# Kernel tuning notes

Measured on AMD Instinct MI355X. Metric: run time of the kernel, lower is better.

Reference implementation:

```python
import jax, jax.numpy as jnp
import numpy as np

N_FRUSTUMS = 14400  # n_splits_azi(360) * n_splits_pol(40)
N_POINTS = 2_000_000
N_CHANNELS = 8


def setup_inputs() -> dict:
    key = jax.random.key(0)
    k1, k2 = jax.random.split(key)
    pc = jax.random.normal(k1, (N_POINTS, N_CHANNELS), dtype=jnp.float32)
    i_frustum = jnp.sort(
        jax.random.randint(k2, (N_POINTS,), 0, N_FRUSTUMS)
    ).astype(jnp.int32)
    i_inv = jnp.arange(N_POINTS, dtype=jnp.int32)  # identity inverse permutation
    counts_padded = jnp.bincount(i_frustum, length=N_FRUSTUMS).astype(jnp.float32)
    return {
        "pc": pc,
        "i_frustum": i_frustum,
        "i_inv": i_inv,
        "counts_padded": counts_padded,
    }


def reference(pc, i_frustum, i_inv, counts_padded):
    """Faithful port of symmetrize_mean / symmetrize_std / symmetrize_max plus the
    gather-broadcast normalize (pc - mean[i_frustum][i_inv]) / std.

    pc:            [N, C] float point features
    i_frustum:     [N]   int point->frustum segment ids (sorted)
    i_inv:         [N]   int inverse permutation applied after gather
    counts_padded: [F]   float per-frustum point counts (0 for empty frustums)
    """
    n_frustums = counts_padded.shape[0]
    nonempty = counts_padded[:, None] != 0.0  # [F, 1]
    safe_counts = jnp.maximum(counts_padded, 1.0)[:, None]  # avoid div-by-zero

    # symmetrize_mean: scatter_add then divide where count != 0
    sums = jax.ops.segment_sum(pc, i_frustum, num_segments=n_frustums)  # [F, C]
    mean = jnp.where(nonempty, sums / safe_counts, sums)

    # symmetrize_std: scatter_add of squared deviation, divide, sqrt where > 0
    dev = pc - mean[i_frustum][i_inv]  # [N, C] gather-broadcast subtract
    var_sums = jax.ops.segment_sum(dev * dev, i_frustum, num_segments=n_frustums)
    var = jnp.where(nonempty, var_sums / safe_counts, var_sums)
    std = jnp.where(var > 0.0, jnp.sqrt(jnp.maximum(var, 0.0)), var)

    # symmetrize_max: scatter_reduce amax onto a zeros-initialized buffer
    # (include_self=True default in torch => result is max(0, segment max))
    frustum_max = jnp.zeros((n_frustums, pc.shape[1]), pc.dtype).at[i_frustum].max(pc)

    # gather-broadcast normalize (decorator_distance_to_mean style, with per-frustum std)
    std_g = std[i_frustum][i_inv]
    pc_norm = dev / jnp.where(std_g > 0.0, std_g, 1.0)

    return mean, std, frustum_max, pc_norm
```

## Files before the change

### kernel.cpp

```cpp
#include <hip/hip_runtime.h>

#define NCH 8
#define CACHE 8

typedef float v4f __attribute__((ext_vector_type(4)));

__device__ __forceinline__ void acc4(const float4& v, float4& sum, float4& sq, float4& mx) {
    sum.x += v.x; sq.x += v.x * v.x; mx.x = fmaxf(mx.x, v.x);
    sum.y += v.y; sq.y += v.y * v.y; mx.y = fmaxf(mx.y, v.y);
    sum.z += v.z; sq.z += v.z * v.z; mx.z = fmaxf(mx.z, v.z);
    sum.w += v.w; sq.w += v.w * v.w; mx.w = fmaxf(mx.w, v.w);
}

__device__ __forceinline__ v4f norm4(const float4& v, const float4& m, const float4& d) {
    v4f o;
    o.x = (v.x - m.x) * d.x;
    o.y = (v.y - m.y) * d.y;
    o.z = (v.z - m.z) * d.z;
    o.w = (v.w - m.w) * d.w;
    return o;
}

__device__ __forceinline__ int wave_lower_bound(const int* __restrict__ a, int n, int key,
                                                int lane) {
    int lo = 0, len = n;
    while (len > 64) {
        int step = (len + 63) >> 6;
        int p = lo + lane * step;
        int v = (p < lo + len) ? a[p] : 0x7fffffff;
        unsigned long long bal = __ballot(v < key);
        int cnt = __popcll(bal);
        if (cnt == 0) return lo;
        int nlo = lo + (cnt - 1) * step + 1;
        int nhi = lo + len;
        int cap = lo + cnt * step;
        if (cnt < 64 && cap < nhi) nhi = cap;
        lo = nlo; len = nhi - nlo;
    }
    int v = (lane < len) ? a[lo + lane] : 0x7fffffff;
    unsigned long long bal = __ballot(v < key);
    return lo + __popcll(bal);
}

__global__ __launch_bounds__(128) void k_fused(
    const float* __restrict__ pc, const int* __restrict__ i_frustum,
    const float* __restrict__ counts, int n, int F,
    float* __restrict__ out_mean, float* __restrict__ out_std,
    float* __restrict__ out_max, float* __restrict__ out_pcn)
{
    const int wid = (blockIdx.x * blockDim.x + threadIdx.x) >> 6;
    if (wid >= F) return;
    const int lane = threadIdx.x & 63;

    const int s = wave_lower_bound(i_frustum, n, wid, lane);
    const float cnt = counts[wid];
    const int e = s + (int)cnt;

    const float4* __restrict__ pc4 = reinterpret_cast<const float4*>(pc);
    v4f* __restrict__ out4 = reinterpret_cast<v4f*>(out_pcn);

    const int b = s * 2, E = e * 2;

    float4 sum = {0.f, 0.f, 0.f, 0.f};
    float4 sq  = {0.f, 0.f, 0.f, 0.f};
    float4 mx  = {0.f, 0.f, 0.f, 0.f};
    float4 c[CACHE];

    int k = b + lane;
    #pragma unroll
    for (int u = 0; u < CACHE; ++u) {
        if (k < E) { c[u] = pc4[k]; acc4(c[u], sum, sq, mx); }
        k += 64;
    }
    for (int kk = k; kk < E; kk += 64) { float4 v = pc4[kk]; acc4(v, sum, sq, mx); }

    #pragma unroll
    for (int m = 2; m <= 32; m <<= 1) {
        sum.x += __shfl_xor(sum.x, m, 64);
        sum.y += __shfl_xor(sum.y, m, 64);
        sum.z += __shfl_xor(sum.z, m, 64);
        sum.w += __shfl_xor(sum.w, m, 64);
        sq.x  += __shfl_xor(sq.x,  m, 64);
        sq.y  += __shfl_xor(sq.y,  m, 64);
        sq.z  += __shfl_xor(sq.z,  m, 64);
        sq.w  += __shfl_xor(sq.w,  m, 64);
        mx.x = fmaxf(mx.x, __shfl_xor(mx.x, m, 64));
        mx.y = fmaxf(mx.y, __shfl_xor(mx.y, m, 64));
        mx.z = fmaxf(mx.z, __shfl_xor(mx.z, m, 64));
        mx.w = fmaxf(mx.w, __shfl_xor(mx.w, m, 64));
    }

    const float invc = 1.0f / fmaxf(cnt, 1.0f);
    float4 mean, sd, dv;
    mean.x = sum.x * invc; mean.y = sum.y * invc; mean.z = sum.z * invc; mean.w = sum.w * invc;
    float vx = fmaxf(sq.x * invc - mean.x * mean.x, 0.0f);
    float vy = fmaxf(sq.y * invc - mean.y * mean.y, 0.0f);
    float vz = fmaxf(sq.z * invc - mean.z * mean.z, 0.0f);
    float vw = fmaxf(sq.w * invc - mean.w * mean.w, 0.0f);
    sd.x = sqrtf(vx); sd.y = sqrtf(vy); sd.z = sqrtf(vz); sd.w = sqrtf(vw);
    dv.x = 1.0f / (sd.x > 0.f ? sd.x : 1.f);
    dv.y = 1.0f / (sd.y > 0.f ? sd.y : 1.f);
    dv.z = 1.0f / (sd.z > 0.f ? sd.z : 1.f);
    dv.w = 1.0f / (sd.w > 0.f ? sd.w : 1.f);

    if (lane < 2) {
        reinterpret_cast<float4*>(out_mean + (size_t)wid * NCH)[lane] = mean;
        reinterpret_cast<float4*>(out_std  + (size_t)wid * NCH)[lane] = sd;
        reinterpret_cast<float4*>(out_max  + (size_t)wid * NCH)[lane] = mx;
    }

    k = b + lane;
    #pragma unroll
    for (int u = 0; u < CACHE; ++u) {
        if (k < E) {
            v4f o = norm4(c[u], mean, dv);
            __builtin_nontemporal_store(o, &out4[k]);
        }
        k += 64;
    }
    for (int kk = k; kk < E; kk += 64) {
        v4f o = norm4(pc4[kk], mean, dv);
        __builtin_nontemporal_store(o, &out4[kk]);
    }
}

extern "C" void kernel_launch(void* const* d_in, const int* in_sizes, int n_in,
                              void* d_out, int out_size, void* d_ws, size_t ws_size,
                              hipStream_t stream) {
    const float* pc        = (const float*)d_in[0];
    const int*   i_frustum = (const int*)d_in[1];
    const float* counts    = (const float*)d_in[3];

    int n = in_sizes[0] / NCH;
    int F = in_sizes[3];

    float* out_mean = (float*)d_out;
    float* out_std  = out_mean + (size_t)F * NCH;
    float* out_max  = out_std  + (size_t)F * NCH;
    float* out_pcn  = out_max  + (size_t)F * NCH;

    int waves_per_block = 128 / 64;
    int blocks = (F + waves_per_block - 1) / waves_per_block;
    k_fused<<<blocks, 128, 0, stream>>>(pc, i_frustum, counts, n, F,
                                        out_mean, out_std, out_max, out_pcn);
}
```

Before: 31.50 us.

## Process two adjacent frustums per wavefront with a larger register cache

Each wavefront now handles two consecutive frustums. It runs one binary search and streams their combined contiguous point range, splitting the accumulation and normalisation per element by a boundary test. The register cache grows from 8 to 12 float4 so the combined range (about 278 points, 556 float4) mostly stays in registers. This halves the binary searches and wave count and gives each wave more contiguous memory work, at the cost of higher register pressure, duplicated reductions and select overhead.

```diff
diff --git a/kernel.cpp b/kernel.cpp
--- a/kernel.cpp
+++ b/kernel.cpp
@@ -1,7 +1,7 @@
 #include <hip/hip_runtime.h>
 
 #define NCH 8
-#define CACHE 8
+#define CACHE 12
 
 typedef float v4f __attribute__((ext_vector_type(4)));
 
@@ -10,15 +10,6 @@
     sum.y += v.y; sq.y += v.y * v.y; mx.y = fmaxf(mx.y, v.y);
     sum.z += v.z; sq.z += v.z * v.z; mx.z = fmaxf(mx.z, v.z);
     sum.w += v.w; sq.w += v.w * v.w; mx.w = fmaxf(mx.w, v.w);
-}
-
-__device__ __forceinline__ v4f norm4(const float4& v, const float4& m, const float4& d) {
-    v4f o;
-    o.x = (v.x - m.x) * d.x;
-    o.y = (v.y - m.y) * d.y;
-    o.z = (v.z - m.z) * d.z;
-    o.w = (v.w - m.w) * d.w;
-    return o;
 }
 
 __device__ __forceinline__ int wave_lower_bound(const int* __restrict__ a, int n, int key,
@@ -42,38 +33,7 @@
     return lo + __popcll(bal);
 }
 
-__global__ __launch_bounds__(128) void k_fused(
-    const float* __restrict__ pc, const int* __restrict__ i_frustum,
-    const float* __restrict__ counts, int n, int F,
-    float* __restrict__ out_mean, float* __restrict__ out_std,
-    float* __restrict__ out_max, float* __restrict__ out_pcn)
-{
-    const int wid = (blockIdx.x * blockDim.x + threadIdx.x) >> 6;
-    if (wid >= F) return;
-    const int lane = threadIdx.x & 63;
-
-    const int s = wave_lower_bound(i_frustum, n, wid, lane);
-    const float cnt = counts[wid];
-    const int e = s + (int)cnt;
-
-    const float4* __restrict__ pc4 = reinterpret_cast<const float4*>(pc);
-    v4f* __restrict__ out4 = reinterpret_cast<v4f*>(out_pcn);
-
-    const int b = s * 2, E = e * 2;
-
-    float4 sum = {0.f, 0.f, 0.f, 0.f};
-    float4 sq  = {0.f, 0.f, 0.f, 0.f};
-    float4 mx  = {0.f, 0.f, 0.f, 0.f};
-    float4 c[CACHE];
-
-    int k = b + lane;
-    #pragma unroll
-    for (int u = 0; u < CACHE; ++u) {
-        if (k < E) { c[u] = pc4[k]; acc4(c[u], sum, sq, mx); }
-        k += 64;
-    }
-    for (int kk = k; kk < E; kk += 64) { float4 v = pc4[kk]; acc4(v, sum, sq, mx); }
-
+__device__ __forceinline__ void wreduce(float4& sum, float4& sq, float4& mx) {
     #pragma unroll
     for (int m = 2; m <= 32; m <<= 1) {
         sum.x += __shfl_xor(sum.x, m, 64);
@@ -89,9 +49,11 @@
         mx.z = fmaxf(mx.z, __shfl_xor(mx.z, m, 64));
         mx.w = fmaxf(mx.w, __shfl_xor(mx.w, m, 64));
     }
+}
 
+__device__ __forceinline__ void mk_stats(const float4& sum, const float4& sq, float cnt,
+                                         float4& mean, float4& sd, float4& dv) {
     const float invc = 1.0f / fmaxf(cnt, 1.0f);
-    float4 mean, sd, dv;
     mean.x = sum.x * invc; mean.y = sum.y * invc; mean.z = sum.z * invc; mean.w = sum.w * invc;
     float vx = fmaxf(sq.x * invc - mean.x * mean.x, 0.0f);
     float vy = fmaxf(sq.y * invc - mean.y * mean.y, 0.0f);
@@ -102,24 +64,95 @@
     dv.y = 1.0f / (sd.y > 0.f ? sd.y : 1.f);
     dv.z = 1.0f / (sd.z > 0.f ? sd.z : 1.f);
     dv.w = 1.0f / (sd.w > 0.f ? sd.w : 1.f);
+}
+
+__global__ __launch_bounds__(128) void k_fused2(
+    const float* __restrict__ pc, const int* __restrict__ i_frustum,
+    const float* __restrict__ counts, int n, int F,
+    float* __restrict__ out_mean, float* __restrict__ out_std,
+    float* __restrict__ out_max, float* __restrict__ out_pcn)
+{
+    const int wid = (blockIdx.x * blockDim.x + threadIdx.x) >> 6;
+    const int f0 = wid * 2;
+    if (f0 >= F) return;
+    const int f1 = f0 + 1;
+    const int lane = threadIdx.x & 63;
+
+    const int s0 = wave_lower_bound(i_frustum, n, f0, lane);
+    const float c0 = counts[f0];
+    const float c1 = (f1 < F) ? counts[f1] : 0.0f;
+    const int e0 = s0 + (int)c0;
+    const int e1 = e0 + (int)c1;
+
+    const float4* __restrict__ pc4 = reinterpret_cast<const float4*>(pc);
+    v4f* __restrict__ out4 = reinterpret_cast<v4f*>(out_pcn);
+
+    const int B = s0 * 2, E0 = e0 * 2, E1 = e1 * 2;
+
+    float4 sum0 = {0,0,0,0}, sq0 = {0,0,0,0}, mx0 = {0,0,0,0};
+    float4 sum1 = {0,0,0,0}, sq1 = {0,0,0,0}, mx1 = {0,0,0,0};
+    float4 c[CACHE];
+
+    int k = B + lane;
+    #pragma unroll
+    for (int u = 0; u < CACHE; ++u) {
+        if (k < E1) c[u] = pc4[k];
+        k += 64;
+    }
+    k = B + lane;
+    #pragma unroll
+    for (int u = 0; u < CACHE; ++u) {
+        if (k < E1) {
+            if (k < E0) acc4(c[u], sum0, sq0, mx0);
+            else        acc4(c[u], sum1, sq1, mx1);
+        }
+        k += 64;
+    }
+    for (int kk = k; kk < E1; kk += 64) {
+        float4 v = pc4[kk];
+        if (kk < E0) acc4(v, sum0, sq0, mx0);
+        else         acc4(v, sum1, sq1, mx1);
+    }
+
+    wreduce(sum0, sq0, mx0);
+    wreduce(sum1, sq1, mx1);
+
+    float4 mean0, sd0, dv0, mean1, sd1, dv1;
+    mk_stats(sum0, sq0, c0, mean0, sd0, dv0);
+    mk_stats(sum1, sq1, c1, mean1, sd1, dv1);
 
     if (lane < 2) {
-        reinterpret_cast<float4*>(out_mean + (size_t)wid * NCH)[lane] = mean;
-        reinterpret_cast<float4*>(out_std  + (size_t)wid * NCH)[lane] = sd;
-        reinterpret_cast<float4*>(out_max  + (size_t)wid * NCH)[lane] = mx;
+        reinterpret_cast<float4*>(out_mean + (size_t)f0 * NCH)[lane] = mean0;
+        reinterpret_cast<float4*>(out_std  + (size_t)f0 * NCH)[lane] = sd0;
+        reinterpret_cast<float4*>(out_max  + (size_t)f0 * NCH)[lane] = mx0;
+    } else if (lane < 4 && f1 < F) {
+        reinterpret_cast<float4*>(out_mean + (size_t)f1 * NCH)[lane & 1] = mean1;
+        reinterpret_cast<float4*>(out_std  + (size_t)f1 * NCH)[lane & 1] = sd1;
+        reinterpret_cast<float4*>(out_max  + (size_t)f1 * NCH)[lane & 1] = mx1;
     }
 
-    k = b + lane;
+    k = B + lane;
     #pragma unroll
     for (int u = 0; u < CACHE; ++u) {
-        if (k < E) {
-            v4f o = norm4(c[u], mean, dv);
+        if (k < E1) {
+            const bool s0b = k < E0;
+            v4f o;
+            o.x = (c[u].x - (s0b ? mean0.x : mean1.x)) * (s0b ? dv0.x : dv1.x);
+            o.y = (c[u].y - (s0b ? mean0.y : mean1.y)) * (s0b ? dv0.y : dv1.y);
+            o.z = (c[u].z - (s0b ? mean0.z : mean1.z)) * (s0b ? dv0.z : dv1.z);
+            o.w = (c[u].w - (s0b ? mean0.w : mean1.w)) * (s0b ? dv0.w : dv1.w);
             __builtin_nontemporal_store(o, &out4[k]);
         }
         k += 64;
     }
-    for (int kk = k; kk < E; kk += 64) {
-        v4f o = norm4(pc4[kk], mean, dv);
+    for (int kk = k; kk < E1; kk += 64) {
+        float4 v = pc4[kk];
+        const bool s0b = kk < E0;
+        v4f o;
+        o.x = (v.x - (s0b ? mean0.x : mean1.x)) * (s0b ? dv0.x : dv1.x);
+        o.y = (v.y - (s0b ? mean0.y : mean1.y)) * (s0b ? dv0.y : dv1.y);
+        o.z = (v.z - (s0b ? mean0.z : mean1.z)) * (s0b ? dv0.z : dv1.z);
+        o.w = (v.w - (s0b ? mean0.w : mean1.w)) * (s0b ? dv0.w : dv1.w);
         __builtin_nontemporal_store(o, &out4[kk]);
     }
 }
@@ -139,8 +172,9 @@
     float* out_max  = out_std  + (size_t)F * NCH;
     float* out_pcn  = out_max  + (size_t)F * NCH;
 
+    int nwaves = (F + 1) / 2;
     int waves_per_block = 128 / 64;
-    int blocks = (F + waves_per_block - 1) / waves_per_block;
-    k_fused<<<blocks, 128, 0, stream>>>(pc, i_frustum, counts, n, F,
-                                        out_mean, out_std, out_max, out_pcn);
+    int blocks = (nwaves + waves_per_block - 1) / waves_per_block;
+    k_fused2<<<blocks, 128, 0, stream>>>(pc, i_frustum, counts, n, F,
+                                         out_mean, out_std, out_max, out_pcn);
 }
```

Result: slower. 37.65 us (+19.5%).
